# Kernel tuning notes

Hardware: AMD Instinct MI355X
Metric: run time of the kernel (lower is better)

## Reference

```python
import jax, jax.numpy as jnp
import numpy as np

NUM_QUBITS = 512
NUM_CORES = 16
CORE_SIZE = 64
HIDDEN = 128
BATCH = 2048


def setup_inputs() -> dict:
    key = jax.random.key(0)
    k1, k2, k3 = jax.random.split(key, 3)
    last_assignment = jax.random.randint(k1, (BATCH, NUM_QUBITS), 0, NUM_CORES, dtype=jnp.int32)
    adjacency = jnp.ones((NUM_CORES, NUM_CORES), dtype=jnp.float32)  # all-to-all core graph
    qubit_embedding = jax.random.normal(k2, (NUM_QUBITS + 1, HIDDEN), dtype=jnp.float32)
    gcn_weight = jax.random.normal(k3, (HIDDEN, HIDDEN), dtype=jnp.float32) * (1.0 / np.sqrt(HIDDEN))
    gcn_bias = jnp.zeros((HIDDEN,), dtype=jnp.float32)
    return {
        'last_assignment': last_assignment,
        'adjacency': adjacency,
        'qubit_embedding': qubit_embedding,
        'gcn_weight': gcn_weight,
        'gcn_bias': gcn_bias,
    }


def reference(last_assignment, adjacency, qubit_embedding, gcn_weight, gcn_bias):
    B, Q = last_assignment.shape
    C = adjacency.shape[0]
    # --- replace the sequential per-qubit scatter loop with a single cumsum ---
    # pos[b,q] = number of earlier qubits assigned to the same core (the loop's
    # running counter idx); core index C (the extra row) always writes slot 0
    # because the loop resets its counter every iteration.
    oh = jax.nn.one_hot(last_assignment, C + 1, dtype=jnp.int32)        # [B,Q,C+1]
    cnt = jnp.cumsum(oh, axis=1)                                        # inclusive counts
    pos = jnp.take_along_axis(cnt, last_assignment[..., None], axis=2)[..., 0] - 1
    pos = jnp.where(last_assignment == C, 0, pos)
    buf = jnp.full((B, C + 1, CORE_SIZE), Q, dtype=jnp.int32)           # padding id = num_qubits
    b_idx = jnp.arange(B)[:, None]
    q_idx = jnp.broadcast_to(jnp.arange(Q, dtype=jnp.int32)[None, :], (B, Q))
    buf = buf.at[b_idx, last_assignment, pos].set(q_idx, mode='drop')
    buf = buf[:, :C, :]                                                 # drop overflow core row
    # --- embedding (padding row forced to zero, as nn.Embedding padding_idx) ---
    tbl = qubit_embedding.at[Q].set(0.0)
    qubit_embs = tbl[buf]                                               # [B,C,core_size,H]
    core_embs = qubit_embs.max(axis=2)                                  # [B,C,H]
    # --- GCNConv(add_self_loops=False): D^{-1/2} A D^{-1/2} (X W^T) + b ---
    deg = adjacency.sum(axis=0)
    dinv = jnp.where(deg > 0, 1.0 / jnp.sqrt(deg), 0.0)
    a_norm = adjacency * dinv[:, None] * dinv[None, :]                  # symmetric norm
    h = jnp.einsum('bch,oh->bco', core_embs, gcn_weight)                # lin (PyG: x @ W^T)
    out = jnp.einsum('ij,bjo->bio', a_norm, h) + gcn_bias               # [B,C,H]
    return out
```

## Files before the change

### kernel.cpp

```cpp
#include <hip/hip_runtime.h>
#include <stdint.h>

typedef unsigned short u16;
typedef unsigned int u32;
typedef unsigned long long u64;

typedef __bf16 bf16x8 __attribute__((ext_vector_type(8)));
typedef float f32x4 __attribute__((ext_vector_type(4)));
typedef u16 u16x8 __attribute__((ext_vector_type(8)));

#define NQ 512
#define NC 16
#define NH 128
#define NB 2048
#define QE_KEYS (513*128)
#define WT_OFF  QE_KEYS
#define GW_ELEMS (128*128)
#define A_OFF (WT_OFF + GW_ELEMS)
#define LSEG 1088
#define ESEG 2304
#define ESTRIDE 136

static __device__ __forceinline__ u16 f2bf_rne(float f){
  u32 u = __float_as_uint(f);
  u += 0x7fffu + ((u>>16)&1u);
  return (u16)(u>>16);
}
static __device__ __forceinline__ u32 pack_rne(float lo, float hi){
  return (u32)f2bf_rne(lo) | ((u32)f2bf_rne(hi)<<16);
}
static __device__ __forceinline__ u16 key_of(float f){
  u16 b = f2bf_rne(f);
  return (b & 0x8000u) ? (u16)~b : (u16)(b | 0x8000u);
}
static __device__ __forceinline__ u16 unkey(u16 k){
  return (k & 0x8000u) ? (u16)(k ^ 0x8000u) : (u16)~k;
}

union Frag { u32 u[4]; uint4 u4; bf16x8 f; };
union U8   { u16x8 v; int w[4]; uint4 u4; u16 h[8]; };

__global__ void prepass_kernel(const float* __restrict__ qe,
                               const float* __restrict__ gw,
                               const float* __restrict__ adj,
                               u16* __restrict__ ws)
{
  if (blockIdx.x == 0) {
    __shared__ float sD[16];
    int t = threadIdx.x;
    if (t < 16) {
      float s = 0.f;
      for (int i = 0; i < 16; ++i) s += adj[i*16 + t];
      sD[t] = (s > 0.f) ? (1.0f / sqrtf(s)) : 0.f;
    }
    __syncthreads();
    int i = t >> 4, jp = (t & 15) * 2;
    float lo = (jp   < 16) ? adj[i*16 + jp]   * sD[i] * sD[jp]   : 0.f;
    float hi = (jp+1 < 16) ? adj[i*16 + jp+1] * sD[i] * sD[jp+1] : 0.f;
    ((u32*)(ws + A_OFF))[t] = pack_rne(lo, hi);
    return;
  }
  int idx = (blockIdx.x - 1) * 256 + threadIdx.x;
  if (idx < QE_KEYS/8) {
    int i8 = idx * 8;
    uint4 o;
    if (i8 >= 512*NH) {
      o.x = 0x80008000u; o.y = 0x80008000u; o.z = 0x80008000u; o.w = 0x80008000u;
    } else {
      const float4* p = (const float4*)(qe + i8);
      float4 a = p[0], b = p[1];
      o.x = (u32)key_of(a.x) | ((u32)key_of(a.y)<<16);
      o.y = (u32)key_of(a.z) | ((u32)key_of(a.w)<<16);
      o.z = (u32)key_of(b.x) | ((u32)key_of(b.y)<<16);
      o.w = (u32)key_of(b.z) | ((u32)key_of(b.w)<<16);
    }
    *(uint4*)(ws + i8) = o;
  } else if (idx < QE_KEYS/8 + GW_ELEMS/8) {
    int j8 = (idx - QE_KEYS/8) * 8;
    const float4* p = (const float4*)(gw + j8);
    float4 a = p[0], b = p[1];
    uint4 o;
    o.x = pack_rne(a.x, a.y); o.y = pack_rne(a.z, a.w);
    o.z = pack_rne(b.x, b.y); o.w = pack_rne(b.z, b.w);
    *(uint4*)(ws + WT_OFF + j8) = o;
  }
}

static __device__ __forceinline__ void wave_reduce_max(U8& A){
  U8 B;
  #pragma unroll
  for (int j = 0; j < 4; ++j) B.w[j] = __shfl_xor(A.w[j], 16);
  A.v = __builtin_elementwise_max(A.v, B.v);
  #pragma unroll
  for (int j = 0; j < 4; ++j) B.w[j] = __shfl_xor(A.w[j], 32);
  A.v = __builtin_elementwise_max(A.v, B.v);
}

__global__ __launch_bounds__(256, 4)
void core_snapshot_kernel(const int* __restrict__ la,
                          const u16* __restrict__ ws,
                          const float* __restrict__ gb,
                          float* __restrict__ outp)
{
  __shared__ __align__(16) u16 sListAll[4*LSEG];
  __shared__ __align__(16) u16 sEAll[4*ESEG];

  const int tid  = threadIdx.x;
  const int lane = tid & 63;
  const int wv   = tid >> 6;
  const int m    = lane & 15;
  const int quad = lane >> 4;
  const int item = blockIdx.x*4 + wv;
  u16* sList = sListAll + wv*LSEG;
  u16* sE    = sEAll    + wv*ESEG;
  const u16* qt = ws;
  const u16* wt = ws + WT_OFF;

  {
    uint4 f = make_uint4(0x02000200u,0x02000200u,0x02000200u,0x02000200u);
    *(uint4*)&sList[lane*16]     = f;
    *(uint4*)&sList[lane*16 + 8] = f;
  }

  int av[8];
  #pragma unroll
  for (int ch = 0; ch < 8; ++ch) av[ch] = la[item*NQ + ch*64 + lane];
  const u64 lmask = (1ull << lane) - 1ull;
  u32 runbase = 0;
  #pragma unroll
  for (int ch = 0; ch < 8; ++ch) {
    u32 cnt = 0, intra = 0;
    #pragma unroll
    for (int c = 0; c < 16; ++c) {
      u64 mk = __ballot(av[ch] == c);
      if (lane == c)    cnt   = (u32)__popcll(mk);
      if (av[ch] == c)  intra = (u32)__popcll(mk & lmask);
    }
    u32 base = (u32)__shfl((int)runbase, av[ch]);
    u32 rank = base + intra;
    if (rank < 64) sList[av[ch]*64 + (rank&3)*16 + (rank>>2)] = (u16)(ch*64 + lane);
    runbase += cnt;
  }
  const u32 cntv = runbase;

  const u16* qb = qt + m*8;
  for (int c = 0; c < 16; ++c) {
    int cnt = __shfl((int)cntv, c);
    U8 S0, S1;
    S0.u4 = *(const uint4*)&sList[c*64 + quad*16];
    S1.u4 = *(const uint4*)&sList[c*64 + quad*16 + 8];
    U8 A; A.v = (u16x8)0;
    {
      U8 T[8];
      #pragma unroll
      for (int k = 0; k < 8; ++k) T[k].u4 = *(const uint4*)(qb + (int)S0.h[k]*NH);
      #pragma unroll
      for (int k = 0; k < 8; ++k) A.v = __builtin_elementwise_max(A.v, T[k].v);
    }
    if (cnt > 32) {
      U8 T[8];
      #pragma unroll
      for (int k = 0; k < 8; ++k) T[k].u4 = *(const uint4*)(qb + (int)S1.h[k]*NH);
      #pragma unroll
      for (int k = 0; k < 8; ++k) A.v = __builtin_elementwise_max(A.v, T[k].v);
    }
    wave_reduce_max(A);
    if (cnt < 64) {
      U8 Z; Z.v = (u16x8)(u16)0x8000u;
      A.v = __builtin_elementwise_max(A.v, Z.v);
    }
    if (quad == 0) {
      uint4 e;
      e.x = (u32)unkey(A.h[0]) | ((u32)unkey(A.h[1])<<16);
      e.y = (u32)unkey(A.h[2]) | ((u32)unkey(A.h[3])<<16);
      e.z = (u32)unkey(A.h[4]) | ((u32)unkey(A.h[5])<<16);
      e.w = (u32)unkey(A.h[6]) | ((u32)unkey(A.h[7])<<16);
      *(uint4*)&sE[c*ESTRIDE + m*8] = e;
    }
  }

  bf16x8 af[4];
  #pragma unroll
  for (int ks = 0; ks < 4; ++ks)
    af[ks] = *(const bf16x8*)&sE[m*ESTRIDE + ks*32 + quad*8];
  Frag anf;
  anf.u4 = *(const uint4*)(ws + A_OFF + m*32 + quad*8);

  #pragma unroll
  for (int t = 0; t < 8; ++t) {
    f32x4 acc = {0.f, 0.f, 0.f, 0.f};
    #pragma unroll
    for (int ks = 0; ks < 4; ++ks) {
      bf16x8 bfr = *(const bf16x8*)(wt + (t*16 + m)*NH + ks*32 + quad*8);
      acc = __builtin_amdgcn_mfma_f32_16x16x32_bf16(af[ks], bfr, acc, 0, 0, 0);
    }
    float d16[4], d32[4], lo[4], hi[4];
    #pragma unroll
    for (int r = 0; r < 4; ++r) {
      d16[r] = __shfl_down(acc[r], 16);
      d32[r] = __shfl_down(acc[r], 32);
    }
    #pragma unroll
    for (int r = 0; r < 4; ++r) {
      lo[r] = (quad == 0) ? acc[r] : d16[r];
      hi[r] = (quad == 0) ? d16[r] : d32[r];
    }
    Frag hb;
    hb.u[0] = pack_rne(lo[0], lo[1]); hb.u[1] = pack_rne(lo[2], lo[3]);
    hb.u[2] = pack_rne(hi[0], hi[1]); hb.u[3] = pack_rne(hi[2], hi[3]);
    if (quad >= 2) { hb.u[0]=0; hb.u[1]=0; hb.u[2]=0; hb.u[3]=0; }
    float biasv = gb[t*16 + m];
    f32x4 o4 = {biasv, biasv, biasv, biasv};
    o4 = __builtin_amdgcn_mfma_f32_16x16x32_bf16(anf.f, hb.f, o4, 0, 0, 0);
    float* op = outp + item*(NC*NH) + t*16 + m;
    #pragma unroll
    for (int r = 0; r < 4; ++r) op[(quad*4 + r)*NH] = o4[r];
  }
}

extern "C" void kernel_launch(void* const* d_in, const int* in_sizes, int n_in,
                              void* d_out, int out_size, void* d_ws, size_t ws_size,
                              hipStream_t stream) {
  const int*   la  = (const int*)d_in[0];
  const float* adj = (const float*)d_in[1];
  const float* qe  = (const float*)d_in[2];
  const float* gw  = (const float*)d_in[3];
  const float* gb  = (const float*)d_in[4];
  float* outp = (float*)d_out;
  u16* ws = (u16*)d_ws;

  int pre_blocks = 1 + (QE_KEYS/8 + GW_ELEMS/8 + 255)/256;
  prepass_kernel<<<pre_blocks, 256, 0, stream>>>(qe, gw, adj, ws);
  core_snapshot_kernel<<<NB/4, 256, 0, stream>>>(la, ws, gb, outp);
}
```

Before: 92.04 us.

## Split each batch item across two waves with shared-memory count exchange

Each batch item is now handled by two waves instead of one. Each wave ranks half of the qubit assignments, and the per-core counts are exchanged through shared memory to combine the ranks. Each wave then gathers and max-reduces 8 of the 16 cores and computes half of the output column tiles. The second gather half is also split into two 16-entry chunks so fewer padding rows are loaded. This doubles the wave count and shortens each wave's critical path, at the cost of three block-wide barriers and twice as many blocks.

Result: no change. 90.45 us (-1.7%).

```diff
diff --git a/kernel.cpp b/kernel.cpp
--- a/kernel.cpp
+++ b/kernel.cpp
@@ -102,33 +102,37 @@
                           const float* __restrict__ gb,
                           float* __restrict__ outp)
 {
-  __shared__ __align__(16) u16 sListAll[4*LSEG];
-  __shared__ __align__(16) u16 sEAll[4*ESEG];
+  __shared__ __align__(16) u16 sListAll[2*LSEG];
+  __shared__ __align__(16) u16 sEAll[2*ESEG];
+  __shared__ int sCnt[2][2][16];
 
   const int tid  = threadIdx.x;
   const int lane = tid & 63;
   const int wv   = tid >> 6;
+  const int it   = wv >> 1;
+  const int tw   = wv & 1;
   const int m    = lane & 15;
   const int quad = lane >> 4;
-  const int item = blockIdx.x*4 + wv;
-  u16* sList = sListAll + wv*LSEG;
-  u16* sE    = sEAll    + wv*ESEG;
+  const int item = blockIdx.x*2 + it;
+  u16* sList = sListAll + it*LSEG;
+  u16* sE    = sEAll    + it*ESEG;
   const u16* qt = ws;
   const u16* wt = ws + WT_OFF;
 
   {
     uint4 f = make_uint4(0x02000200u,0x02000200u,0x02000200u,0x02000200u);
-    *(uint4*)&sList[lane*16]     = f;
-    *(uint4*)&sList[lane*16 + 8] = f;
-  }
-
-  int av[8];
-  #pragma unroll
-  for (int ch = 0; ch < 8; ++ch) av[ch] = la[item*NQ + ch*64 + lane];
+    *(uint4*)&sList[tw*512 + lane*8] = f;
+  }
+  __syncthreads();
+
+  int av[4];
+  #pragma unroll
+  for (int ch = 0; ch < 4; ++ch) av[ch] = la[item*NQ + (tw*4 + ch)*64 + lane];
   const u64 lmask = (1ull << lane) - 1ull;
   u32 runbase = 0;
-  #pragma unroll
-  for (int ch = 0; ch < 8; ++ch) {
+  u32 rankrel[4];
+  #pragma unroll
+  for (int ch = 0; ch < 4; ++ch) {
     u32 cnt = 0, intra = 0;
     #pragma unroll
     for (int c = 0; c < 16; ++c) {
@@ -137,14 +141,34 @@
       if (av[ch] == c)  intra = (u32)__popcll(mk & lmask);
     }
     u32 base = (u32)__shfl((int)runbase, av[ch]);
-    u32 rank = base + intra;
-    if (rank < 64) sList[av[ch]*64 + (rank&3)*16 + (rank>>2)] = (u16)(ch*64 + lane);
+    rankrel[ch] = base + intra;
     runbase += cnt;
   }
-  const u32 cntv = runbase;
+  if (lane < 16) sCnt[it][tw][lane] = (int)runbase;
+  if (tw == 0) {
+    #pragma unroll
+    for (int ch = 0; ch < 4; ++ch) {
+      u32 rank = rankrel[ch];
+      if (rank < 64) sList[av[ch]*64 + (rank&3)*16 + (rank>>2)] = (u16)(ch*64 + lane);
+    }
+  }
+  __syncthreads();
+  u32 cntv;
+  if (tw == 1) {
+    #pragma unroll
+    for (int ch = 0; ch < 4; ++ch) {
+      u32 rank = (u32)sCnt[it][0][av[ch]] + rankrel[ch];
+      if (rank < 64) sList[av[ch]*64 + (rank&3)*16 + (rank>>2)] = (u16)((4 + ch)*64 + lane);
+    }
+    cntv = runbase + (u32)((lane < 16) ? sCnt[it][0][lane] : 0);
+  } else {
+    cntv = runbase + (u32)((lane < 16) ? sCnt[it][1][lane] : 0);
+  }
+  __syncthreads();
 
   const u16* qb = qt + m*8;
-  for (int c = 0; c < 16; ++c) {
+  for (int cc = 0; cc < 8; ++cc) {
+    int c = tw*8 + cc;
     int cnt = __shfl((int)cntv, c);
     U8 S0, S1;
     S0.u4 = *(const uint4*)&sList[c*64 + quad*16];
@@ -158,11 +182,18 @@
       for (int k = 0; k < 8; ++k) A.v = __builtin_elementwise_max(A.v, T[k].v);
     }
     if (cnt > 32) {
-      U8 T[8];
-      #pragma unroll
-      for (int k = 0; k < 8; ++k) T[k].u4 = *(const uint4*)(qb + (int)S1.h[k]*NH);
-      #pragma unroll
-      for (int k = 0; k < 8; ++k) A.v = __builtin_elementwise_max(A.v, T[k].v);
+      U8 T[4];
+      #pragma unroll
+      for (int k = 0; k < 4; ++k) T[k].u4 = *(const uint4*)(qb + (int)S1.h[k]*NH);
+      #pragma unroll
+      for (int k = 0; k < 4; ++k) A.v = __builtin_elementwise_max(A.v, T[k].v);
+    }
+    if (cnt > 48) {
+      U8 T[4];
+      #pragma unroll
+      for (int k = 0; k < 4; ++k) T[k].u4 = *(const uint4*)(qb + (int)S1.h[4+k]*NH);
+      #pragma unroll
+      for (int k = 0; k < 4; ++k) A.v = __builtin_elementwise_max(A.v, T[k].v);
     }
     wave_reduce_max(A);
     if (cnt < 64) {
@@ -178,6 +209,7 @@
       *(uint4*)&sE[c*ESTRIDE + m*8] = e;
     }
   }
+  __syncthreads();
 
   bf16x8 af[4];
   #pragma unroll
@@ -187,7 +219,8 @@
   anf.u4 = *(const uint4*)(ws + A_OFF + m*32 + quad*8);
 
   #pragma unroll
-  for (int t = 0; t < 8; ++t) {
+  for (int tt = 0; tt < 4; ++tt) {
+    int t = tw*4 + tt;
     f32x4 acc = {0.f, 0.f, 0.f, 0.f};
     #pragma unroll
     for (int ks = 0; ks < 4; ++ks) {
@@ -231,5 +264,5 @@
 
   int pre_blocks = 1 + (QE_KEYS/8 + GW_ELEMS/8 + 255)/256;
   prepass_kernel<<<pre_blocks, 256, 0, stream>>>(qe, gw, adj, ws);
-  core_snapshot_kernel<<<NB/4, 256, 0, stream>>>(la, ws, gb, outp);
-}
+  core_snapshot_kernel<<<NB/2, 256, 0, stream>>>(la, ws, gb, outp);
+}
```
